# Optimization experiments

Measured on AMD Instinct MI355X. Metric: run time of the kernel, lower is better.

## Reference

```python
import jax, jax.numpy as jnp
import numpy as np

B, IMG, P, C_IN, D, NH, DEPTH, E, TOPK, NCLS = 8, 224, 16, 3, 768, 12, 12, 8, 2, 1000
DH = 4 * D
HD = D // NH
GRID = IMG // P
NPAT = GRID * GRID
MOE_POS = (1, 3, 5, 7, 9, 11)
N_DENSE = DEPTH - len(MOE_POS)
N_MOE = len(MOE_POS)


def setup_inputs() -> dict:
    key = jax.random.key(0)
    ks = iter(jax.random.split(key, 32))
    n = lambda shape: jax.random.normal(next(ks), shape, jnp.float32) * 0.02
    return dict(
        x=jax.random.normal(next(ks), (B, C_IN, IMG, IMG), jnp.float32),
        patch_w=n((D, C_IN * P * P)), patch_b=jnp.zeros((D,), jnp.float32),
        cls_token=n((1, 1, D)), pos_embed=n((1, NPAT + 1, D)),
        ln1_w=jnp.ones((DEPTH, D), jnp.float32), ln1_b=jnp.zeros((DEPTH, D), jnp.float32),
        qkv_w=n((DEPTH, 3 * D, D)), qkv_b=jnp.zeros((DEPTH, 3 * D), jnp.float32),
        proj_w=n((DEPTH, D, D)), proj_b=jnp.zeros((DEPTH, D), jnp.float32),
        ln2_w=jnp.ones((DEPTH, D), jnp.float32), ln2_b=jnp.zeros((DEPTH, D), jnp.float32),
        fc1_w=n((N_DENSE, DH, D)), fc1_b=jnp.zeros((N_DENSE, DH), jnp.float32),
        fc2_w=n((N_DENSE, D, DH)), fc2_b=jnp.zeros((N_DENSE, D), jnp.float32),
        gate_w=n((N_MOE, E, D)), gate_b=jnp.zeros((N_MOE, E), jnp.float32),
        exp_w1=n((N_MOE, E, DH, D)), exp_b1=jnp.zeros((N_MOE, E, DH), jnp.float32),
        exp_w2=n((N_MOE, E, D, DH)), exp_b2=jnp.zeros((N_MOE, E, D), jnp.float32),
        norm_w=jnp.ones((D,), jnp.float32), norm_b=jnp.zeros((D,), jnp.float32),
        head_w=n((NCLS, D)), head_b=jnp.zeros((NCLS,), jnp.float32),
    )


def _ln(x, w, b):
    m = x.mean(-1, keepdims=True)
    v = ((x - m) ** 2).mean(-1, keepdims=True)
    return (x - m) / jnp.sqrt(v + 1e-5) * w + b


def _attn(x, qw, qb, pw, pb):
    Bn, N, _ = x.shape
    qkv = (x @ qw.T + qb).reshape(Bn, N, 3, NH, HD).transpose(2, 0, 3, 1, 4)
    q, k, v = qkv[0], qkv[1], qkv[2]  # [B, NH, N, HD]
    a = jax.nn.softmax(jnp.einsum('bhnd,bhmd->bhnm', q, k) * HD ** -0.5, -1)
    o = jnp.einsum('bhnm,bhmd->bhnd', a, v).transpose(0, 2, 1, 3).reshape(Bn, N, D)
    return o @ pw.T + pb


def _moe(x, gw, gb, w1, b1, w2, b2):
    # FMoETransformerMLP with NaiveGate: top-2 routing, softmax over top-k logits.
    shp = x.shape
    xf = x.reshape(-1, D)  # [T, D]
    logits = xf @ gw.T + gb  # [T, E]
    vals, idx = jax.lax.top_k(logits, TOPK)
    sc = jax.nn.softmax(vals, -1)  # [T, TOPK]
    comb = (jax.nn.one_hot(idx, E, dtype=xf.dtype) * sc[..., None]).sum(1)  # [T, E]
    h = jax.nn.gelu(jnp.einsum('td,ehd->teh', xf, w1) + b1, approximate=False)
    y = jnp.einsum('teh,edh->ted', h, w2) + b2
    return (y * comb[..., None]).sum(1).reshape(shp)


def reference(x, patch_w, patch_b, cls_token, pos_embed, ln1_w, ln1_b, qkv_w, qkv_b, proj_w, proj_b, ln2_w, ln2_b, fc1_w, fc1_b, fc2_w, fc2_b, gate_w, gate_b, exp_w1, exp_b1, exp_w2, exp_b2, norm_w, norm_b, head_w, head_b):
    patches = x.reshape(B, C_IN, GRID, P, GRID, P).transpose(0, 2, 4, 1, 3, 5).reshape(B, NPAT, C_IN * P * P)
    z = jnp.concatenate([jnp.broadcast_to(cls_token, (B, 1, D)), patches @ patch_w.T + patch_b], 1) + pos_embed
    di = mi = 0
    for i in range(DEPTH):
        z = z + _attn(_ln(z, ln1_w[i], ln1_b[i]), qkv_w[i], qkv_b[i], proj_w[i], proj_b[i])
        h2 = _ln(z, ln2_w[i], ln2_b[i])
        if i in MOE_POS:
            z = z + _moe(h2, gate_w[mi], gate_b[mi], exp_w1[mi], exp_b1[mi], exp_w2[mi], exp_b2[mi])
            mi += 1
        else:
            z = z + (jax.nn.gelu(h2 @ fc1_w[di].T + fc1_b[di], approximate=False) @ fc2_w[di].T + fc2_b[di])
            di += 1
    z = _ln(z, norm_w, norm_b)
    return z[:, 0] @ head_w.T + head_b
```

## Files before the change

kernel.cpp:

```cpp
#include <hip/hip_runtime.h>
#include <hip/hip_bf16.h>
#include <math.h>

#define B_     8
#define IMG_   224
#define PATCH_ 16
#define CIN_   3
#define D_     768
#define NH_    12
#define DEPTH_ 12
#define NE_    8
#define NCLS_  1000
#define DH_    3072
#define HD_    64
#define GRD_   14
#define NPAT_  196
#define NTOK_  197
#define T_     (B_*NTOK_)
#define TP_    (B_*NPAT_)
#define NSLOT_ (T_*2)

typedef __bf16 bf16_t;
typedef __bf16 bf16x8 __attribute__((ext_vector_type(8)));
typedef __bf16 bf16x4 __attribute__((ext_vector_type(4)));
typedef float  f32x4  __attribute__((ext_vector_type(4)));

static __device__ __forceinline__ float gelu_f(float x){
    return 0.5f * x * (1.0f + erff(x * 0.70710678118654752440f));
}

__global__ __launch_bounds__(256) void k_cvt(const float* __restrict__ in,
                                             bf16_t* __restrict__ out, int n){
    int i = (blockIdx.x*256 + threadIdx.x)*8;
    if (i >= n) return;
    float4 a = *reinterpret_cast<const float4*>(in + i);
    float4 b = *reinterpret_cast<const float4*>(in + i + 4);
    bf16x8 h;
    h[0]=(bf16_t)a.x; h[1]=(bf16_t)a.y; h[2]=(bf16_t)a.z; h[3]=(bf16_t)a.w;
    h[4]=(bf16_t)b.x; h[5]=(bf16_t)b.y; h[6]=(bf16_t)b.z; h[7]=(bf16_t)b.w;
    *reinterpret_cast<bf16x8*>(out + i) = h;
}

__global__ void k_patch_gather(const float* __restrict__ x, bf16_t* __restrict__ pbuf){
    int idx = blockIdx.x*256 + threadIdx.x;
    if (idx >= TP_*D_) return;
    int k  = idx % D_;
    int tp = idx / D_;
    int p  = tp % NPAT_, b = tp / NPAT_;
    int c  = k >> 8;
    int ij = k & 255;
    int i  = ij >> 4, j = ij & 15;
    int gi = p / GRD_, gj = p % GRD_;
    pbuf[idx] = (bf16_t)x[(((size_t)b*CIN_ + c)*IMG_ + gi*PATCH_ + i)*IMG_ + gj*PATCH_ + j];
}

template<int ACT, int GATHER, int MOE, int OUTBF, int KSPLIT, int PARTIAL>
__global__ __launch_bounds__(256) void k_mgemm(
    const bf16_t* __restrict__ A, const int* __restrict__ gidx,
    const bf16_t* __restrict__ W, const float* __restrict__ bias,
    void* __restrict__ Cout, int M, int N, int K,
    const int* __restrict__ moff, const int* __restrict__ mcnt)
{
    __shared__ __align__(16) bf16_t As[2][64*64];
    __shared__ __align__(16) bf16_t Bs[2][128*64];
    const int tid = threadIdx.x, lane = tid & 63, w = tid >> 6;
    int row_begin, Mhi, ksid;
    if (MOE) {
        const int e = blockIdx.z;
        const int o = moff[e], c = mcnt[e];
        const int rb = (KSPLIT == 2) ? (int)(blockIdx.y >> 1) : (int)blockIdx.y;
        ksid = (KSPLIT == 2) ? (int)(blockIdx.y & 1) : 0;
        row_begin = o + rb*64;
        Mhi = o + c;
        if (row_begin >= Mhi) return;
        W += (size_t)e*N*K;
        if (!PARTIAL) bias += (size_t)e*N;
    } else {
        row_begin = blockIdx.y*64;
        ksid = (KSPLIT == 2) ? (int)blockIdx.z : 0;
        Mhi = M;
    }
    const int bn = blockIdx.x*128;
    const int KL = K / KSPLIT;

    const bf16_t* aG[2];
    const bf16_t* wG[4];
    int aOff[2], wOff[4];
    #pragma unroll
    for (int i = 0; i < 2; ++i) {
        const int s = w*2 + i;
        const int row_l = s*8 + (lane >> 3);
        const int cc = (lane & 7) ^ (row_l & 7);
        const int gg = min(row_begin + row_l, Mhi - 1);
        const int tok = GATHER ? (gidx[gg] >> 1) : gg;
        aG[i] = A + (size_t)tok*K + ksid*KL + cc*8;
        aOff[i] = s*512;
    }
    #pragma unroll
    for (int j = 0; j < 4; ++j) {
        const int s = w*4 + j;
        const int row_l = s*8 + (lane >> 3);
        const int cc = (lane & 7) ^ (row_l & 7);
        wG[j] = W + (size_t)(bn + row_l)*K + ksid*KL + cc*8;
        wOff[j] = s*512;
    }
    const int wm = (w >> 1)*32, wn = (w & 1)*64;
    const int fr = lane & 15, kg = lane >> 4;
    int offA[2][2], offB[2][4];
    #pragma unroll
    for (int ks = 0; ks < 2; ++ks) {
        #pragma unroll
        for (int t = 0; t < 2; ++t) {
            const int ra = wm + t*16 + fr;
            offA[ks][t] = ra*128 + (((ks*4 + kg) ^ (ra & 7)) << 4);
        }
        #pragma unroll
        for (int t = 0; t < 4; ++t) {
            const int rb2 = wn + t*16 + fr;
            offB[ks][t] = rb2*128 + (((ks*4 + kg) ^ (rb2 & 7)) << 4);
        }
    }

    f32x4 acc[2][4] = {};
    const int nt = KL >> 6;
    int cur = 0;
    #pragma unroll
    for (int i = 0; i < 2; ++i) {
        __builtin_amdgcn_global_load_lds(
            (const __attribute__((address_space(1))) void*)(aG[i]),
            (__attribute__((address_space(3))) void*)(&As[0][aOff[i]]), 16, 0, 0);
        aG[i] += 64;
    }
    #pragma unroll
    for (int j = 0; j < 4; ++j) {
        __builtin_amdgcn_global_load_lds(
            (const __attribute__((address_space(1))) void*)(wG[j]),
            (__attribute__((address_space(3))) void*)(&Bs[0][wOff[j]]), 16, 0, 0);
        wG[j] += 64;
    }
    __syncthreads();
    for (int t = 0; t < nt; ++t) {
        if (t + 1 < nt) {
            const int nb = cur ^ 1;
            #pragma unroll
            for (int i = 0; i < 2; ++i) {
                __builtin_amdgcn_global_load_lds(
                    (const __attribute__((address_space(1))) void*)(aG[i]),
                    (__attribute__((address_space(3))) void*)(&As[nb][aOff[i]]), 16, 0, 0);
                aG[i] += 64;
            }
            #pragma unroll
            for (int j = 0; j < 4; ++j) {
                __builtin_amdgcn_global_load_lds(
                    (const __attribute__((address_space(1))) void*)(wG[j]),
                    (__attribute__((address_space(3))) void*)(&Bs[nb][wOff[j]]), 16, 0, 0);
                wG[j] += 64;
            }
        }
        const char* baseA = (const char*)&As[cur][0];
        const char* baseB = (const char*)&Bs[cur][0];
        #pragma unroll
        for (int ks = 0; ks < 2; ++ks) {
            bf16x8 af[2], bf[4];
            #pragma unroll
            for (int t2 = 0; t2 < 2; ++t2)
                af[t2] = *reinterpret_cast<const bf16x8*>(baseA + offA[ks][t2]);
            #pragma unroll
            for (int t2 = 0; t2 < 4; ++t2)
                bf[t2] = *reinterpret_cast<const bf16x8*>(baseB + offB[ks][t2]);
            #pragma unroll
            for (int mt = 0; mt < 2; ++mt)
                #pragma unroll
                for (int nt2 = 0; nt2 < 4; ++nt2)
                    acc[mt][nt2] = __builtin_amdgcn_mfma_f32_16x16x32_bf16(
                        af[mt], bf[nt2], acc[mt][nt2], 0, 0, 0);
        }
        __syncthreads();
        cur ^= 1;
    }
    float*  Cf = (float*)Cout + ((PARTIAL && KSPLIT == 2) ? (size_t)ksid*M*N : (size_t)0);
    bf16_t* Cb = (bf16_t*)Cout;
    const int cr = kg*4;
    #pragma unroll
    for (int nt2 = 0; nt2 < 4; ++nt2) {
        const int n = bn + wn + nt2*16 + fr;
        const float bv = PARTIAL ? 0.0f : bias[n];
        #pragma unroll
        for (int mt = 0; mt < 2; ++mt) {
            #pragma unroll
            for (int r2 = 0; r2 < 4; ++r2) {
                const int m = row_begin + wm + mt*16 + cr + r2;
                if (m < Mhi) {
                    float v = acc[mt][nt2][r2] + bv;
                    if (ACT) v = gelu_f(v);
                    if (OUTBF) Cb[(size_t)m*N + n] = (bf16_t)v;
                    else       Cf[(size_t)m*N + n] = v;
                }
            }
        }
    }
}

struct LNOut { float y0, y1, y2; };
static __device__ __forceinline__ LNOut ln_block(float v0, float v1, float v2,
        const float* __restrict__ w, const float* __restrict__ b,
        float* red, int tid)
{
    const int wid = tid >> 6, lane = tid & 63;
    float s = v0 + v1 + v2;
    for (int m=32;m>0;m>>=1) s += __shfl_xor(s, m);
    if (lane == 0) red[wid] = s;
    __syncthreads();
    if (tid == 0) red[4] = (red[0]+red[1]+red[2]+red[3]) * (1.0f/768.0f);
    __syncthreads();
    const float mean = red[4];
    float d0 = v0-mean, d1 = v1-mean, d2 = v2-mean;
    float q = d0*d0 + d1*d1 + d2*d2;
    for (int m=32;m>0;m>>=1) q += __shfl_xor(q, m);
    if (lane == 0) red[wid] = q;
    __syncthreads();
    if (tid == 0) {
        float var = (red[0]+red[1]+red[2]+red[3]) * (1.0f/768.0f);
        red[5] = 1.0f / sqrtf(var + 1e-5f);
    }
    __syncthreads();
    const float rstd = red[5];
    LNOut o;
    o.y0 = d0*rstd*w[tid    ] + b[tid    ];
    o.y1 = d1*rstd*w[tid+256] + b[tid+256];
    o.y2 = d2*rstd*w[tid+512] + b[tid+512];
    return o;
}

template<typename TOUT>
__global__ __launch_bounds__(256) void k_ln(const float* __restrict__ X,
        const float* __restrict__ w, const float* __restrict__ b,
        TOUT* __restrict__ Y, int in_mul)
{
    __shared__ float red[8];
    const int r = blockIdx.x, tid = threadIdx.x;
    const float* xr = X + (size_t)r*in_mul*D_;
    LNOut o = ln_block(xr[tid], xr[tid+256], xr[tid+512], w, b, red, tid);
    TOUT* yr = Y + (size_t)r*D_;
    yr[tid] = (TOUT)o.y0; yr[tid+256] = (TOUT)o.y1; yr[tid+512] = (TOUT)o.y2;
}

__global__ __launch_bounds__(256) void k_asmln(const float* __restrict__ pe,
        const float* __restrict__ cls, const float* __restrict__ pos,
        float* __restrict__ z, const float* __restrict__ w,
        const float* __restrict__ b, bf16_t* __restrict__ Y)
{
    __shared__ float red[8];
    const int t = blockIdx.x, tid = threadIdx.x;
    const int bb = t / NTOK_, r = t % NTOK_;
    float v[3];
    #pragma unroll
    for (int j = 0; j < 3; ++j) {
        const int n = tid + j*256;
        if (r == 0) v[j] = cls[n] + pos[n];
        else        v[j] = pe[((size_t)bb*NPAT_ + (r-1))*D_ + n] + pos[(size_t)r*D_ + n];
        z[(size_t)t*D_ + n] = v[j];
    }
    LNOut o = ln_block(v[0], v[1], v[2], w, b, red, tid);
    bf16_t* yr = Y + (size_t)t*D_;
    yr[tid] = (bf16_t)o.y0; yr[tid+256] = (bf16_t)o.y1; yr[tid+512] = (bf16_t)o.y2;
}

template<int GATE, int NP>
__global__ __launch_bounds__(256) void k_addln(
    float* __restrict__ z, const float* __restrict__ P,
    const float* __restrict__ bias,
    const float* __restrict__ w, const float* __restrict__ b,
    bf16_t* __restrict__ Y,
    const float* __restrict__ gw, const float* __restrict__ gb,
    int* __restrict__ t_e, float* __restrict__ t_sc)
{
    __shared__ float red[8];
    __shared__ float red2[4][8];
    const int t = blockIdx.x, tid = threadIdx.x;
    const int wid = tid >> 6, lane = tid & 63;
    const float* P1 = P + (size_t)T_*D_;
    float v[3];
    #pragma unroll
    for (int j = 0; j < 3; ++j) {
        const int n = tid + j*256;
        float nv = z[(size_t)t*D_+n] + P[(size_t)t*D_+n] + bias[n];
        if (NP == 2) nv += P1[(size_t)t*D_+n];
        z[(size_t)t*D_+n] = nv;
        v[j] = nv;
    }
    LNOut o = ln_block(v[0], v[1], v[2], w, b, red, tid);
    bf16_t* yr = Y + (size_t)t*D_;
    yr[tid] = (bf16_t)o.y0; yr[tid+256] = (bf16_t)o.y1; yr[tid+512] = (bf16_t)o.y2;
    if (GATE) {
        float p[NE_];
        #pragma unroll
        for (int e = 0; e < NE_; ++e)
            p[e] = o.y0*gw[e*D_+tid] + o.y1*gw[e*D_+tid+256] + o.y2*gw[e*D_+tid+512];
        #pragma unroll
        for (int e = 0; e < NE_; ++e)
            for (int m=32;m>0;m>>=1) p[e] += __shfl_xor(p[e], m);
        if (lane == 0)
            #pragma unroll
            for (int e = 0; e < NE_; ++e) red2[wid][e] = p[e];
        __syncthreads();
        if (tid == 0) {
            float l[NE_];
            #pragma unroll
            for (int e = 0; e < NE_; ++e)
                l[e] = red2[0][e]+red2[1][e]+red2[2][e]+red2[3][e] + gb[e];
            int i0 = 0;
            for (int e = 1; e < NE_; ++e) if (l[e] > l[i0]) i0 = e;
            int i1 = -1;
            for (int e = 0; e < NE_; ++e) if (e != i0 && (i1 < 0 || l[e] > l[i1])) i1 = e;
            float e1 = __expf(l[i1] - l[i0]);
            float s = 1.0f + e1;
            t_e[t*2]   = i0;   t_e[t*2+1]  = i1;
            t_sc[t*2]  = 1.0f/s; t_sc[t*2+1] = e1/s;
        }
    }
}

__global__ __launch_bounds__(1024) void k_scansc(const int* __restrict__ t_e,
        int* __restrict__ gidx, int* __restrict__ rg,
        int* __restrict__ offs, int* __restrict__ counts)
{
    __shared__ int h[NE_], o[NE_], c2[NE_];
    const int tid = threadIdx.x;
    if (tid < NE_) h[tid] = 0;
    __syncthreads();
    for (int id = tid; id < NSLOT_; id += 1024) atomicAdd(&h[t_e[id]], 1);
    __syncthreads();
    if (tid == 0) {
        int s = 0;
        for (int e = 0; e < NE_; ++e) { o[e] = s; s += h[e]; c2[e] = 0; }
    }
    __syncthreads();
    if (tid < NE_) { offs[tid] = o[tid]; counts[tid] = h[tid]; }
    for (int id = tid; id < NSLOT_; id += 1024) {
        int e = t_e[id];
        int pos = atomicAdd(&c2[e], 1);
        int g = o[e] + pos;
        gidx[g] = id;
        rg[id] = g;
    }
}

template<int LN>
__global__ __launch_bounds__(256) void k_comb(
    const float* __restrict__ mp, const float* __restrict__ b2,
    const int* __restrict__ t_e, const int* __restrict__ rg,
    const float* __restrict__ t_sc, float* __restrict__ z,
    const float* __restrict__ w, const float* __restrict__ b,
    bf16_t* __restrict__ Y)
{
    __shared__ float red[8];
    const int t = blockIdx.x, tid = threadIdx.x;
    const int g0 = rg[2*t], g1 = rg[2*t+1];
    const int e0 = t_e[2*t], e1 = t_e[2*t+1];
    const float s0 = t_sc[2*t], s1 = t_sc[2*t+1];
    const float* mp1 = mp + (size_t)NSLOT_*D_;
    float v[3];
    #pragma unroll
    for (int j = 0; j < 3; ++j) {
        const int n = tid + j*256;
        float y0 = mp[(size_t)g0*D_+n] + mp1[(size_t)g0*D_+n] + b2[(size_t)e0*D_+n];
        float y1 = mp[(size_t)g1*D_+n] + mp1[(size_t)g1*D_+n] + b2[(size_t)e1*D_+n];
        float nv = z[(size_t)t*D_+n] + s0*y0 + s1*y1;
        z[(size_t)t*D_+n] = nv;
        v[j] = nv;
    }
    if (LN) {
        LNOut o = ln_block(v[0], v[1], v[2], w, b, red, tid);
        bf16_t* yr = Y + (size_t)t*D_;
        yr[tid] = (bf16_t)o.y0; yr[tid+256] = (bf16_t)o.y1; yr[tid+512] = (bf16_t)o.y2;
    }
}

__global__ __launch_bounds__(256) void k_attn(const bf16_t* __restrict__ qkv,
                                              bf16_t* __restrict__ out)
{
    __shared__ bf16_t Kl[NTOK_*68];
    __shared__ float  qs[8][64];
    __shared__ bf16_t ps[8][200];
    const int qb = blockIdx.x*8;
    const int h = blockIdx.y, b = blockIdx.z;
    const int tid = threadIdx.x, lane = tid & 63, wid = tid >> 6;
    for (int id = tid; id < NTOK_*8; id += 256) {
        const int m = id >> 3, c = id & 7;
        bf16x8 v = *reinterpret_cast<const bf16x8*>(
            qkv + (size_t)(b*NTOK_+m)*2304 + 768 + h*HD_ + c*8);
        bf16x4 lo = {v[0],v[1],v[2],v[3]}, hi = {v[4],v[5],v[6],v[7]};
        *reinterpret_cast<bf16x4*>(&Kl[m*68 + c*8    ]) = lo;
        *reinterpret_cast<bf16x4*>(&Kl[m*68 + c*8 + 4]) = hi;
    }
    for (int id = tid; id < 512; id += 256) {
        const int qq = id >> 6, d = id & 63;
        const int n = qb + qq;
        qs[qq][d] = (n < NTOK_) ? (float)qkv[(size_t)(b*NTOK_+n)*2304 + h*HD_ + d] : 0.0f;
    }
    __syncthreads();
    const int na = qb + wid, nb = qb + wid + 4;
    const bool va = na < NTOK_, vb = nb < NTOK_;
    if (!va) return;
    float sa[4] = {0,0,0,0}, sb[4] = {0,0,0,0};
    for (int d = 0; d < HD_; d += 4) {
        const f32x4 qa = *reinterpret_cast<const f32x4*>(&qs[wid][d]);
        const f32x4 qv = *reinterpret_cast<const f32x4*>(&qs[wid+4][d]);
        #pragma unroll
        for (int j = 0; j < 4; ++j) {
            const int m = lane + 64*j;
            const int mc = m < NTOK_ ? m : NTOK_-1;
            bf16x4 kv = *reinterpret_cast<const bf16x4*>(&Kl[mc*68 + d]);
            float k0=(float)kv[0], k1=(float)kv[1], k2=(float)kv[2], k3=(float)kv[3];
            sa[j] += qa[0]*k0 + qa[1]*k1 + qa[2]*k2 + qa[3]*k3;
            sb[j] += qv[0]*k0 + qv[1]*k1 + qv[2]*k2 + qv[3]*k3;
        }
    }
    #pragma unroll
    for (int j = 0; j < 4; ++j) {
        const bool ok = (lane + 64*j) < NTOK_;
        sa[j] = ok ? sa[j]*0.125f : -3.0e38f;
        sb[j] = ok ? sb[j]*0.125f : -3.0e38f;
    }
    float mxa = fmaxf(fmaxf(sa[0],sa[1]), fmaxf(sa[2],sa[3]));
    float mxb = fmaxf(fmaxf(sb[0],sb[1]), fmaxf(sb[2],sb[3]));
    for (int m=32;m>0;m>>=1) { mxa = fmaxf(mxa, __shfl_xor(mxa,m)); mxb = fmaxf(mxb, __shfl_xor(mxb,m)); }
    float pa[4], pb[4], suma = 0.0f, sumb = 0.0f;
    #pragma unroll
    for (int j = 0; j < 4; ++j) {
        pa[j] = __expf(sa[j]-mxa); suma += pa[j];
        pb[j] = __expf(sb[j]-mxb); sumb += pb[j];
    }
    for (int m=32;m>0;m>>=1) { suma += __shfl_xor(suma,m); sumb += __shfl_xor(sumb,m); }
    #pragma unroll
    for (int j = 0; j < 4; ++j) {
        const int m = lane + 64*j;
        if (m < NTOK_) {
            ps[wid][m] = (bf16_t)pa[j];
            if (vb) ps[wid+4][m] = (bf16_t)pb[j];
        }
    }
    const float inva = 1.0f/suma, invb = 1.0f/sumb;
    const bf16_t* vbase = qkv + (size_t)b*NTOK_*2304 + 1536 + h*HD_ + lane;
    float aa = 0.0f, ab = 0.0f;
    if (vb) {
        for (int m = 0; m < NTOK_; ++m) {
            const float vv = (float)vbase[(size_t)m*2304];
            aa += (float)ps[wid][m]*vv;
            ab += (float)ps[wid+4][m]*vv;
        }
    } else {
        for (int m = 0; m < NTOK_; ++m)
            aa += (float)ps[wid][m]*(float)vbase[(size_t)m*2304];
    }
    out[(size_t)(b*NTOK_+na)*D_ + h*HD_ + lane] = (bf16_t)(aa*inva);
    if (vb) out[(size_t)(b*NTOK_+nb)*D_ + h*HD_ + lane] = (bf16_t)(ab*invb);
}

__global__ __launch_bounds__(256) void k_head(const float* __restrict__ zn,
        const float* __restrict__ hw, const float* __restrict__ hb,
        float* __restrict__ out)
{
    const int o = blockIdx.x*4 + (threadIdx.x >> 6);
    const int b = blockIdx.y;
    const int lane = threadIdx.x & 63;
    if (o >= NCLS_) return;
    float acc = 0.0f;
    #pragma unroll 4
    for (int k = lane; k < D_; k += 64)
        acc = fmaf(zn[b*D_+k], hw[(size_t)o*D_+k], acc);
    for (int m=32;m>0;m>>=1) acc += __shfl_xor(acc, m);
    if (lane == 0) out[b*NCLS_+o] = acc + hb[o];
}

extern "C" void kernel_launch(void* const* d_in, const int* in_sizes, int n_in,
                              void* d_out, int out_size, void* d_ws, size_t ws_size,
                              hipStream_t stream)
{
    const float* x        = (const float*)d_in[0];
    const float* patch_w  = (const float*)d_in[1];
    const float* patch_b  = (const float*)d_in[2];
    const float* cls_tok  = (const float*)d_in[3];
    const float* pos_emb  = (const float*)d_in[4];
    const float* ln1_w    = (const float*)d_in[5];
    const float* ln1_b    = (const float*)d_in[6];
    const float* qkv_w    = (const float*)d_in[7];
    const float* qkv_b    = (const float*)d_in[8];
    const float* proj_w   = (const float*)d_in[9];
    const float* proj_b   = (const float*)d_in[10];
    const float* ln2_w    = (const float*)d_in[11];
    const float* ln2_b    = (const float*)d_in[12];
    const float* fc1_w    = (const float*)d_in[13];
    const float* fc1_b    = (const float*)d_in[14];
    const float* fc2_w    = (const float*)d_in[15];
    const float* fc2_b    = (const float*)d_in[16];
    const float* gate_w   = (const float*)d_in[17];
    const float* gate_b   = (const float*)d_in[18];
    const float* exp_w1   = (const float*)d_in[19];
    const float* exp_b1   = (const float*)d_in[20];
    const float* exp_w2   = (const float*)d_in[21];
    const float* exp_b2   = (const float*)d_in[22];
    const float* norm_w   = (const float*)d_in[23];
    const float* norm_b   = (const float*)d_in[24];
    const float* head_w   = (const float*)d_in[25];
    const float* head_b   = (const float*)d_in[26];

    char* wsb = (char*)d_ws;
    size_t off_ = 0;
    auto alloc = [&](size_t nelem, size_t esz) -> void* {
        void* p = wsb + off_;
        off_ += ((nelem*esz + 255) / 256) * 256;
        return p;
    };
    float*  z      = (float*) alloc((size_t)T_*D_, 4);
    bf16_t* lnbuf  = (bf16_t*)alloc((size_t)T_*D_, 2);
    bf16_t* qkvbuf = (bf16_t*)alloc((size_t)T_*3*D_, 2);
    bf16_t* abuf   = (bf16_t*)alloc((size_t)T_*D_, 2);
    bf16_t* hid    = (bf16_t*)alloc((size_t)NSLOT_*DH_, 2);
    float*  pp     = (float*) alloc((size_t)2*T_*D_, 4);
    float*  mp     = (float*) alloc((size_t)2*NSLOT_*D_, 4);
    float*  t_sc   = (float*) alloc(NSLOT_, 4);
    float*  zn     = (float*) alloc((size_t)B_*D_, 4);
    int*    t_e    = (int*)   alloc(NSLOT_, 4);
    int*    rg     = (int*)   alloc(NSLOT_, 4);
    int*    gidx   = (int*)   alloc(NSLOT_, 4);
    int*    offs   = (int*)   alloc(8, 4);
    int*    counts = (int*)   alloc(8, 4);
    const size_t n_patch = (size_t)D_*D_;
    const size_t n_qkv   = (size_t)DEPTH_*3*D_*D_;
    const size_t n_proj  = (size_t)DEPTH_*D_*D_;
    const size_t n_fc1   = (size_t)6*DH_*D_;
    const size_t n_fc2   = (size_t)6*D_*DH_;
    const size_t n_e1    = (size_t)6*NE_*DH_*D_;
    const size_t n_e2    = (size_t)6*NE_*D_*DH_;
    bf16_t* wb_patch = (bf16_t*)alloc(n_patch, 2);
    bf16_t* wb_qkv   = (bf16_t*)alloc(n_qkv, 2);
    bf16_t* wb_proj  = (bf16_t*)alloc(n_proj, 2);
    bf16_t* wb_fc1   = (bf16_t*)alloc(n_fc1, 2);
    bf16_t* wb_fc2   = (bf16_t*)alloc(n_fc2, 2);
    bf16_t* wb_e1    = (bf16_t*)alloc(n_e1, 2);
    bf16_t* wb_e2    = (bf16_t*)alloc(n_e2, 2);
    bf16_t* pbuf   = hid;
    float*  pout   = mp;

    auto cvt = [&](const float* src, bf16_t* dst, size_t n){
        k_cvt<<<dim3((unsigned)((n/8 + 255)/256)), 256, 0, stream>>>(src, dst, (int)n);
    };
    cvt(patch_w, wb_patch, n_patch);
    cvt(qkv_w,   wb_qkv,   n_qkv);
    cvt(proj_w,  wb_proj,  n_proj);
    cvt(fc1_w,   wb_fc1,   n_fc1);
    cvt(fc2_w,   wb_fc2,   n_fc2);
    cvt(exp_w1,  wb_e1,    n_e1);
    cvt(exp_w2,  wb_e2,    n_e2);

    k_patch_gather<<<dim3((TP_*D_+255)/256), 256, 0, stream>>>(x, pbuf);
    k_mgemm<0,0,0,0,1,0><<<dim3(D_/128, (TP_+63)/64), 256, 0, stream>>>(
        pbuf, nullptr, wb_patch, patch_b, pout, TP_, D_, D_, nullptr, nullptr);
    k_asmln<<<T_, 256, 0, stream>>>(pout, cls_tok, pos_emb, z, ln1_w, ln1_b, lnbuf);

    const int GY = (T_+63)/64;
    int di = 0, mi = 0;
    for (int i = 0; i < DEPTH_; ++i){
        k_mgemm<0,0,0,1,1,0><<<dim3(3*D_/128, GY), 256, 0, stream>>>(
            lnbuf, nullptr, wb_qkv + (size_t)i*3*D_*D_, qkv_b + (size_t)i*3*D_,
            qkvbuf, T_, 3*D_, D_, nullptr, nullptr);
        k_attn<<<dim3((NTOK_+7)/8, NH_, B_), 256, 0, stream>>>(qkvbuf, abuf);
        k_mgemm<0,0,0,0,1,1><<<dim3(D_/128, GY), 256, 0, stream>>>(
            abuf, nullptr, wb_proj + (size_t)i*D_*D_, nullptr,
            pp, T_, D_, D_, nullptr, nullptr);
        if (i & 1){
            k_addln<1,1><<<T_, 256, 0, stream>>>(z, pp, proj_b + i*D_,
                ln2_w + i*D_, ln2_b + i*D_, lnbuf,
                gate_w + (size_t)mi*NE_*D_, gate_b + (size_t)mi*NE_, t_e, t_sc);
            k_scansc<<<1, 1024, 0, stream>>>(t_e, gidx, rg, offs, counts);
            k_mgemm<1,1,1,1,1,0><<<dim3(DH_/128, 50, NE_), 256, 0, stream>>>(
                lnbuf, gidx, wb_e1 + (size_t)mi*NE_*DH_*D_, exp_b1 + (size_t)mi*NE_*DH_,
                hid, NSLOT_, DH_, D_, offs, counts);
            k_mgemm<0,0,1,0,2,1><<<dim3(D_/128, 100, NE_), 256, 0, stream>>>(
                hid, nullptr, wb_e2 + (size_t)mi*NE_*D_*DH_, nullptr,
                mp, NSLOT_, D_, DH_, offs, counts);
            if (i + 1 < DEPTH_) {
                k_comb<1><<<T_, 256, 0, stream>>>(mp, exp_b2 + (size_t)mi*NE_*D_,
                    t_e, rg, t_sc, z, ln1_w + (i+1)*D_, ln1_b + (i+1)*D_, lnbuf);
            } else {
                k_comb<0><<<T_, 256, 0, stream>>>(mp, exp_b2 + (size_t)mi*NE_*D_,
                    t_e, rg, t_sc, z, nullptr, nullptr, nullptr);
            }
            mi++;
        } else {
            k_addln<0,1><<<T_, 256, 0, stream>>>(z, pp, proj_b + i*D_,
                ln2_w + i*D_, ln2_b + i*D_, lnbuf,
                nullptr, nullptr, nullptr, nullptr);
            k_mgemm<1,0,0,1,1,0><<<dim3(DH_/128, GY), 256, 0, stream>>>(
                lnbuf, nullptr, wb_fc1 + (size_t)di*DH_*D_, fc1_b + (size_t)di*DH_,
                hid, T_, DH_, D_, nullptr, nullptr);
            k_mgemm<0,0,0,0,2,1><<<dim3(D_/128, GY, 2), 256, 0, stream>>>(
                hid, nullptr, wb_fc2 + (size_t)di*D_*DH_, nullptr,
                pp, T_, D_, DH_, nullptr, nullptr);
            k_addln<0,2><<<T_, 256, 0, stream>>>(z, pp, fc2_b + di*D_,
                ln1_w + (i+1)*D_, ln1_b + (i+1)*D_, lnbuf,
                nullptr, nullptr, nullptr, nullptr);
            di++;
        }
    }
    k_ln<float><<<B_, 256, 0, stream>>>(z, norm_w, norm_b, zn, NTOK_);
    k_head<<<dim3((NCLS_+3)/4, B_), 256, 0, stream>>>(zn, head_w, head_b, (float*)d_out);
}
```

Measured before the change: 2.626 ms.

## Triple-buffer GEMM LDS tiles with vmcnt-based waits and a single barrier

Changes the k_mgemm main loop from double to triple buffering of the A/W tiles in LDS. Loads are issued two tiles ahead, and each iteration waits on the vmcnt counter so only the current tile's loads must land, followed by one s_barrier instead of two __syncthreads. This hides more global-load latency and removes a barrier per iteration. In exchange, LDS use grows from 48KB to 72KB per block, which may cut occupancy, and correctness now relies on the hand-set vmcnt(6) matching the six loads issued per tile.

```diff
diff --git a/kernel.cpp b/kernel.cpp
--- a/kernel.cpp
+++ b/kernel.cpp
@@ -61,8 +61,8 @@
     void* __restrict__ Cout, int M, int N, int K,
     const int* __restrict__ moff, const int* __restrict__ mcnt)
 {
-    __shared__ __align__(16) bf16_t As[2][64*64];
-    __shared__ __align__(16) bf16_t Bs[2][128*64];
+    __shared__ __align__(16) bf16_t As[3][64*64];
+    __shared__ __align__(16) bf16_t Bs[3][128*64];
     const int tid = threadIdx.x, lane = tid & 63, w = tid >> 6;
     int row_begin, Mhi, ksid;
     if (MOE) {
@@ -121,42 +121,35 @@
         }
     }
 
+    auto issue = [&](int sb) {
+        #pragma unroll
+        for (int i = 0; i < 2; ++i) {
+            __builtin_amdgcn_global_load_lds(
+                (const __attribute__((address_space(1))) void*)(aG[i]),
+                (__attribute__((address_space(3))) void*)(&As[sb][aOff[i]]), 16, 0, 0);
+            aG[i] += 64;
+        }
+        #pragma unroll
+        for (int j = 0; j < 4; ++j) {
+            __builtin_amdgcn_global_load_lds(
+                (const __attribute__((address_space(1))) void*)(wG[j]),
+                (__attribute__((address_space(3))) void*)(&Bs[sb][wOff[j]]), 16, 0, 0);
+            wG[j] += 64;
+        }
+    };
+
     f32x4 acc[2][4] = {};
     const int nt = KL >> 6;
-    int cur = 0;
-    #pragma unroll
-    for (int i = 0; i < 2; ++i) {
-        __builtin_amdgcn_global_load_lds(
-            (const __attribute__((address_space(1))) void*)(aG[i]),
-            (__attribute__((address_space(3))) void*)(&As[0][aOff[i]]), 16, 0, 0);
-        aG[i] += 64;
-    }
-    #pragma unroll
-    for (int j = 0; j < 4; ++j) {
-        __builtin_amdgcn_global_load_lds(
-            (const __attribute__((address_space(1))) void*)(wG[j]),
-            (__attribute__((address_space(3))) void*)(&Bs[0][wOff[j]]), 16, 0, 0);
-        wG[j] += 64;
-    }
-    __syncthreads();
+    issue(0);
+    if (nt > 1) issue(1);
+    int cur = 0, nxt2 = 2;
     for (int t = 0; t < nt; ++t) {
-        if (t + 1 < nt) {
-            const int nb = cur ^ 1;
-            #pragma unroll
-            for (int i = 0; i < 2; ++i) {
-                __builtin_amdgcn_global_load_lds(
-                    (const __attribute__((address_space(1))) void*)(aG[i]),
-                    (__attribute__((address_space(3))) void*)(&As[nb][aOff[i]]), 16, 0, 0);
-                aG[i] += 64;
-            }
-            #pragma unroll
-            for (int j = 0; j < 4; ++j) {
-                __builtin_amdgcn_global_load_lds(
-                    (const __attribute__((address_space(1))) void*)(wG[j]),
-                    (__attribute__((address_space(3))) void*)(&Bs[nb][wOff[j]]), 16, 0, 0);
-                wG[j] += 64;
-            }
-        }
+        if (t + 1 < nt) { asm volatile("s_waitcnt vmcnt(6)" ::: "memory"); }
+        else            { asm volatile("s_waitcnt vmcnt(0)" ::: "memory"); }
+        __builtin_amdgcn_sched_barrier(0);
+        __builtin_amdgcn_s_barrier();
+        __builtin_amdgcn_sched_barrier(0);
+        if (t + 2 < nt) issue(nxt2);
         const char* baseA = (const char*)&As[cur][0];
         const char* baseB = (const char*)&Bs[cur][0];
         #pragma unroll
@@ -175,8 +168,8 @@
                     acc[mt][nt2] = __builtin_amdgcn_mfma_f32_16x16x32_bf16(
                         af[mt], bf[nt2], acc[mt][nt2], 0, 0, 0);
         }
-        __syncthreads();
-        cur ^= 1;
+        cur  = (cur  == 2) ? 0 : cur  + 1;
+        nxt2 = (nxt2 == 2) ? 0 : nxt2 + 1;
     }
     float*  Cf = (float*)Cout + ((PARTIAL && KSPLIT == 2) ? (size_t)ksid*M*N : (size_t)0);
     bf16_t* Cb = (bf16_t*)Cout;
```

Measured after the change: 2.897 ms. 1.1x slower.

## Add dense GEMM kernel with 128-wide K tiles for non-MoE matmuls

Applied to the files above, without the earlier changes.

Introduces k_dgemm, a dense-only GEMM that loads 128-element K tiles per stage straight into LDS with global_load_lds and no double buffering. It replaces the generic k_mgemm for the QKV, projection, and dense MLP GEMMs. The goal is to halve the number of K iterations and barriers and to drop the gather/expert indexing overhead. In exchange it uses a single LDS buffer with a larger footprint (48KB), which may lower occupancy and exposes load latency with no overlap.

```diff
diff --git a/kernel.cpp b/kernel.cpp
--- a/kernel.cpp
+++ b/kernel.cpp
@@ -177,6 +177,120 @@
         }
         __syncthreads();
         cur ^= 1;
+    }
+    float*  Cf = (float*)Cout + ((PARTIAL && KSPLIT == 2) ? (size_t)ksid*M*N : (size_t)0);
+    bf16_t* Cb = (bf16_t*)Cout;
+    const int cr = kg*4;
+    #pragma unroll
+    for (int nt2 = 0; nt2 < 4; ++nt2) {
+        const int n = bn + wn + nt2*16 + fr;
+        const float bv = PARTIAL ? 0.0f : bias[n];
+        #pragma unroll
+        for (int mt = 0; mt < 2; ++mt) {
+            #pragma unroll
+            for (int r2 = 0; r2 < 4; ++r2) {
+                const int m = row_begin + wm + mt*16 + cr + r2;
+                if (m < Mhi) {
+                    float v = acc[mt][nt2][r2] + bv;
+                    if (ACT) v = gelu_f(v);
+                    if (OUTBF) Cb[(size_t)m*N + n] = (bf16_t)v;
+                    else       Cf[(size_t)m*N + n] = v;
+                }
+            }
+        }
+    }
+}
+
+template<int ACT, int OUTBF, int KSPLIT, int PARTIAL>
+__global__ __launch_bounds__(256) void k_dgemm(
+    const bf16_t* __restrict__ A,
+    const bf16_t* __restrict__ W, const float* __restrict__ bias,
+    void* __restrict__ Cout, int M, int N, int K)
+{
+    __shared__ __align__(16) bf16_t As[64*128];
+    __shared__ __align__(16) bf16_t Bs[128*128];
+    const int tid = threadIdx.x, lane = tid & 63, w = tid >> 6;
+    const int row_begin = blockIdx.y*64;
+    const int ksid = (KSPLIT == 2) ? (int)blockIdx.z : 0;
+    const int Mhi = M;
+    const int bn = blockIdx.x*128;
+    const int KL = K / KSPLIT;
+
+    const bf16_t* aG[4];
+    int aOff[4];
+    #pragma unroll
+    for (int i = 0; i < 4; ++i) {
+        const int s = w*4 + i;
+        const int row_l = s*4 + (lane >> 4);
+        const int cc = (lane & 15) ^ (row_l & 7);
+        const int gg = min(row_begin + row_l, Mhi - 1);
+        aG[i] = A + (size_t)gg*K + ksid*KL + cc*8;
+        aOff[i] = s*512;
+    }
+    const bf16_t* wG[8];
+    int wOff[8];
+    #pragma unroll
+    for (int j = 0; j < 8; ++j) {
+        const int s = w*8 + j;
+        const int row_l = s*4 + (lane >> 4);
+        const int cc = (lane & 15) ^ (row_l & 7);
+        wG[j] = W + (size_t)(bn + row_l)*K + ksid*KL + cc*8;
+        wOff[j] = s*512;
+    }
+    const int wm = (w >> 1)*32, wn = (w & 1)*64;
+    const int fr = lane & 15, kg = lane >> 4;
+    int offA[4][2], offB[4][4];
+    #pragma unroll
+    for (int ks = 0; ks < 4; ++ks) {
+        #pragma unroll
+        for (int t = 0; t < 2; ++t) {
+            const int ra = wm + t*16 + fr;
+            offA[ks][t] = ra*256 + (((ks*4 + kg) ^ (ra & 7)) << 4);
+        }
+        #pragma unroll
+        for (int t = 0; t < 4; ++t) {
+            const int rb2 = wn + t*16 + fr;
+            offB[ks][t] = rb2*256 + (((ks*4 + kg) ^ (rb2 & 7)) << 4);
+        }
+    }
+
+    f32x4 acc[2][4] = {};
+    const int nt = KL >> 7;
+    for (int t = 0; t < nt; ++t) {
+        if (t) __syncthreads();
+        #pragma unroll
+        for (int i = 0; i < 4; ++i) {
+            __builtin_amdgcn_global_load_lds(
+                (const __attribute__((address_space(1))) void*)(aG[i]),
+                (__attribute__((address_space(3))) void*)(&As[aOff[i]]), 16, 0, 0);
+            aG[i] += 128;
+        }
+        #pragma unroll
+        for (int j = 0; j < 8; ++j) {
+            __builtin_amdgcn_global_load_lds(
+                (const __attribute__((address_space(1))) void*)(wG[j]),
+                (__attribute__((address_space(3))) void*)(&Bs[wOff[j]]), 16, 0, 0);
+            wG[j] += 128;
+        }
+        __syncthreads();
+        const char* baseA = (const char*)&As[0];
+        const char* baseB = (const char*)&Bs[0];
+        #pragma unroll
+        for (int ks = 0; ks < 4; ++ks) {
+            bf16x8 af[2], bf[4];
+            #pragma unroll
+            for (int t2 = 0; t2 < 2; ++t2)
+                af[t2] = *reinterpret_cast<const bf16x8*>(baseA + offA[ks][t2]);
+            #pragma unroll
+            for (int t2 = 0; t2 < 4; ++t2)
+                bf[t2] = *reinterpret_cast<const bf16x8*>(baseB + offB[ks][t2]);
+            #pragma unroll
+            for (int mt = 0; mt < 2; ++mt)
+                #pragma unroll
+                for (int nt2 = 0; nt2 < 4; ++nt2)
+                    acc[mt][nt2] = __builtin_amdgcn_mfma_f32_16x16x32_bf16(
+                        af[mt], bf[nt2], acc[mt][nt2], 0, 0, 0);
+        }
     }
     float*  Cf = (float*)Cout + ((PARTIAL && KSPLIT == 2) ? (size_t)ksid*M*N : (size_t)0);
     bf16_t* Cb = (bf16_t*)Cout;
@@ -563,13 +677,13 @@
     const int GY = (T_+63)/64;
     int di = 0, mi = 0;
     for (int i = 0; i < DEPTH_; ++i){
-        k_mgemm<0,0,0,1,1,0><<<dim3(3*D_/128, GY), 256, 0, stream>>>(
-            lnbuf, nullptr, wb_qkv + (size_t)i*3*D_*D_, qkv_b + (size_t)i*3*D_,
-            qkvbuf, T_, 3*D_, D_, nullptr, nullptr);
+        k_dgemm<0,1,1,0><<<dim3(3*D_/128, GY), 256, 0, stream>>>(
+            lnbuf, wb_qkv + (size_t)i*3*D_*D_, qkv_b + (size_t)i*3*D_,
+            qkvbuf, T_, 3*D_, D_);
         k_attn<<<dim3((NTOK_+7)/8, NH_, B_), 256, 0, stream>>>(qkvbuf, abuf);
-        k_mgemm<0,0,0,0,1,1><<<dim3(D_/128, GY), 256, 0, stream>>>(
-            abuf, nullptr, wb_proj + (size_t)i*D_*D_, nullptr,
-            pp, T_, D_, D_, nullptr, nullptr);
+        k_dgemm<0,0,1,1><<<dim3(D_/128, GY), 256, 0, stream>>>(
+            abuf, wb_proj + (size_t)i*D_*D_, nullptr,
+            pp, T_, D_, D_);
         if (i & 1){
             k_addln<1,1><<<T_, 256, 0, stream>>>(z, pp, proj_b + i*D_,
                 ln2_w + i*D_, ln2_b + i*D_, lnbuf,
@@ -593,12 +707,12 @@
             k_addln<0,1><<<T_, 256, 0, stream>>>(z, pp, proj_b + i*D_,
                 ln2_w + i*D_, ln2_b + i*D_, lnbuf,
                 nullptr, nullptr, nullptr, nullptr);
-            k_mgemm<1,0,0,1,1,0><<<dim3(DH_/128, GY), 256, 0, stream>>>(
-                lnbuf, nullptr, wb_fc1 + (size_t)di*DH_*D_, fc1_b + (size_t)di*DH_,
-                hid, T_, DH_, D_, nullptr, nullptr);
-            k_mgemm<0,0,0,0,2,1><<<dim3(D_/128, GY, 2), 256, 0, stream>>>(
-                hid, nullptr, wb_fc2 + (size_t)di*D_*DH_, nullptr,
-                pp, T_, D_, DH_, nullptr, nullptr);
+            k_dgemm<1,1,1,0><<<dim3(DH_/128, GY), 256, 0, stream>>>(
+                lnbuf, wb_fc1 + (size_t)di*DH_*D_, fc1_b + (size_t)di*DH_,
+                hid, T_, DH_, D_);
+            k_dgemm<0,0,2,1><<<dim3(D_/128, GY, 2), 256, 0, stream>>>(
+                hid, wb_fc2 + (size_t)di*D_*DH_, nullptr,
+                pp, T_, D_, DH_);
             k_addln<0,2><<<T_, 256, 0, stream>>>(z, pp, fc2_b + di*D_,
                 ln1_w + (i+1)*D_, ln1_b + (i+1)*D_, lnbuf,
                 nullptr, nullptr, nullptr, nullptr);
```

Result: faster. 2.534 ms (-3.5%).
